# Kernel optimization log

Measured on AMD Instinct MI355X. Metric: run time of the kernel, lower is better.

## Reference

```python
import jax, jax.numpy as jnp
import numpy as np

N, F, S, D, H, K, L = 6000, 16, 64, 256, 8, 32, 2
DH = D // H
NEG = jnp.float32(-1e9)


def _ln(x, g, b, eps=1e-5):
    m = jnp.mean(x, axis=-1, keepdims=True)
    v = jnp.var(x, axis=-1, keepdims=True)
    return (x - m) * jax.lax.rsqrt(v + eps) * g + b


def _gelu(x):
    return jax.nn.gelu(x, approximate=False)  # torch nn.GELU default = exact erf


def setup_inputs() -> dict:
    keys = iter(jax.random.split(jax.random.key(0), 64))

    def p(*shape):
        return jax.random.normal(next(keys), shape, jnp.float32) * 0.02

    return dict(
        x=jax.random.normal(next(keys), (N, F, S), jnp.float32),
        gru_Wih=p(F, 3 * D, S), gru_bih=p(F, 3 * D), gru_bhh=p(F, 3 * D),
        va_Wq=p(L, D, D), va_bq=p(L, D), va_Wk=p(L, D, D), va_bk=p(L, D),
        va_Wv=p(L, D, D), va_bv=p(L, D),
        va_lnq_g=jnp.ones((L, D)), va_lnq_b=jnp.zeros((L, D)),
        va_lnk_g=jnp.ones((L, D)), va_lnk_b=jnp.zeros((L, D)),
        va_lnv_g=jnp.ones((L, D)), va_lnv_b=jnp.zeros((L, D)),
        va_Wo=p(L, D, D), va_bo=p(L, D),
        va_ln_g=jnp.ones((L, D)), va_ln_b=jnp.zeros((L, D)),
        va_fi_W1=p(L, D, D), va_fi_b1=p(L, D), va_fi_W2=p(L, D), va_fi_b2=p(L),
        gat_W=p(3, D, D), gat_asrc=p(3, H, DH), gat_adst=p(3, H, DH), gat_bias=p(3, D),
        imp_W=p(3, D), imp_b=p(3),
        ga_ln_g=jnp.ones((D,)), ga_ln_b=jnp.zeros((D,)),
        fin_ln_g=jnp.ones((D,)), fin_ln_b=jnp.zeros((D,)),
        pred_W1=p(D, 2 * D), pred_b1=p(2 * D), pred_W2=p(2 * D), pred_b2=p(),
    )


def _gat(x, W, asrc, adst, bias, src, tgt, valid):
    # PyG GATConv (concat heads, leaky_relu slope 0.2); messages flow src -> tgt.
    # PyG removes then re-adds self loops; `valid` masks removed self-duplicates,
    # the last N edges are the re-added self loops.
    h = (x @ W).reshape(N, H, DH)                              # [N,H,DH]
    es = jnp.einsum('nhd,hd->nh', h, asrc)
    ed = jnp.einsum('nhd,hd->nh', h, adst)
    e = jax.nn.leaky_relu(es[src] + ed[tgt], 0.2)              # [E,H]
    e = jnp.where(valid[:, None], e, NEG)
    m = jax.ops.segment_max(e, tgt, num_segments=N)            # [N,H]
    p = jnp.where(valid[:, None], jnp.exp(e - m[tgt]), 0.0)
    s = jax.ops.segment_sum(p, tgt, num_segments=N)
    alpha = p / (s[tgt] + 1e-16)                               # segment softmax
    out = jax.ops.segment_sum(alpha[:, :, None] * h[src], tgt, num_segments=N)
    return out.reshape(N, D) + bias


def _forward(x, gru_Wih, gru_bih, gru_bhh, va_Wq, va_bq, va_Wk, va_bk, va_Wv, va_bv,
             va_lnq_g, va_lnq_b, va_lnk_g, va_lnk_b, va_lnv_g, va_lnv_b,
             va_Wo, va_bo, va_ln_g, va_ln_b, va_fi_W1, va_fi_b1, va_fi_W2, va_fi_b2,
             gat_W, gat_asrc, gat_adst, gat_bias, imp_W, imp_b,
             ga_ln_g, ga_ln_b, fin_ln_g, fin_ln_b, pred_W1, pred_b1, pred_W2, pred_b2):
    # --- TimeMixing ('gru'): single-step GRU cell per feature, h0 = 0 (torch gate order r,z,n)
    g = jnp.einsum('nfs,fks->nfk', x, gru_Wih) + gru_bih       # [N,F,3D]
    gr, gz, gn = jnp.split(g, 3, axis=-1)
    br, bz, bn = jnp.split(gru_bhh, 3, axis=-1)
    r = jax.nn.sigmoid(gr + br)
    z = jax.nn.sigmoid(gz + bz)
    emb = (1.0 - z) * jnp.tanh(gn + r * bn)                    # [N,F,D]

    # --- VariableAttentionLayers (attention over the F feature tokens, batch = nodes)
    scale = 1.0 / np.sqrt(DH)
    fi = None
    for l in range(L):
        xo = emb
        q = _ln(emb @ va_Wq[l] + va_bq[l], va_lnq_g[l], va_lnq_b[l]).reshape(N, F, H, DH)
        kk = _ln(emb @ va_Wk[l] + va_bk[l], va_lnk_g[l], va_lnk_b[l]).reshape(N, F, H, DH)
        vv = _ln(emb @ va_Wv[l] + va_bv[l], va_lnv_g[l], va_lnv_b[l]).reshape(N, F, H, DH)
        A = jax.nn.softmax(jnp.einsum('bche,bshe->bhcs', q, kk) * scale, axis=-1)
        o = jnp.einsum('bhcs,bshd->bchd', A, vv).reshape(N, F, D) @ va_Wo[l] + va_bo[l]
        emb = _ln(_gelu(o) + xo, va_ln_g[l], va_ln_b[l])
        w = _gelu(emb @ va_fi_W1[l] + va_fi_b1[l]) @ va_fi_W2[l] + va_fi_b2[l]  # [N,F]
        fi = jax.nn.softmax(w, axis=1)[..., None]              # softmax over features

    # --- FeatureImportanceTokenizedBlock
    node = jnp.sum(fi * emb, axis=1)                           # [N,D]

    # --- top-k / bottom-k neighbor selection (cosine similarity, self excluded)
    xn = node * jax.lax.rsqrt(jnp.sum(node * node, axis=-1, keepdims=True) + 1e-12)
    sim = xn @ xn.T                                            # [N,N]
    diag = jnp.eye(N, dtype=bool)
    _, top_idx = jax.lax.top_k(jnp.where(diag, NEG, sim), K)   # [N,K]
    _, bot_idx = jax.lax.top_k(jnp.where(diag, NEG, -sim), K)  # [N,K]

    rng = jnp.arange(N)

    def edges(idx):
        s0 = jnp.repeat(rng, K)
        t0 = idx.reshape(-1)
        src = jnp.concatenate([s0, rng])
        tgt = jnp.concatenate([t0, rng])
        valid = jnp.concatenate([s0 != t0, jnp.ones((N,), bool)])
        return src, tgt, valid

    # --- GatedAttentionLayer: self GAT has only self loops -> attention weight = 1
    self_out = node @ gat_W[0] + gat_bias[0]
    s1, t1, m1 = edges(top_idx)
    top_out = _gat(node, gat_W[1], gat_asrc[1], gat_adst[1], gat_bias[1], s1, t1, m1)
    s2, t2, m2 = edges(bot_idx)
    bot_out = _gat(node, gat_W[2], gat_asrc[2], gat_adst[2], gat_bias[2], s2, t2, m2)

    logits = jnp.stack([self_out @ imp_W[0] + imp_b[0],
                        top_out @ imp_W[1] + imp_b[1],
                        bot_out @ imp_W[2] + imp_b[2]], axis=-1)  # [N,3]
    iw = jax.nn.softmax(logits, axis=-1)
    fused = iw[:, 0:1] * self_out + iw[:, 1:2] * top_out + iw[:, 2:3] * bot_out
    out = _ln(_gelu(fused) + node, ga_ln_g, ga_ln_b)

    # --- final norm + predictor
    out = _ln(out, fin_ln_g, fin_ln_b)
    pred = _gelu(out @ pred_W1 + pred_b1) @ pred_W2 + pred_b2
    return pred[:, None]                                       # [N,1]


def reference(x, gru_Wih, gru_bih, gru_bhh, va_Wq, va_bq, va_Wk, va_bk, va_Wv, va_bv,
              va_lnq_g, va_lnq_b, va_lnk_g, va_lnk_b, va_lnv_g, va_lnv_b,
              va_Wo, va_bo, va_ln_g, va_ln_b, va_fi_W1, va_fi_b1, va_fi_W2, va_fi_b2,
              gat_W, gat_asrc, gat_adst, gat_bias, imp_W, imp_b,
              ga_ln_g, ga_ln_b, fin_ln_g, fin_ln_b, pred_W1, pred_b1, pred_W2, pred_b2):
    return _forward(x, gru_Wih, gru_bih, gru_bhh, va_Wq, va_bq, va_Wk, va_bk, va_Wv, va_bv,
                    va_lnq_g, va_lnq_b, va_lnk_g, va_lnk_b, va_lnv_g, va_lnv_b,
                    va_Wo, va_bo, va_ln_g, va_ln_b, va_fi_W1, va_fi_b1, va_fi_W2, va_fi_b2,
                    gat_W, gat_asrc, gat_adst, gat_bias, imp_W, imp_b,
                    ga_ln_g, ga_ln_b, fin_ln_g, fin_ln_b, pred_W1, pred_b1, pred_W2, pred_b2)
```

## Files before the change

### kernel.cpp

```cpp
#include <hip/hip_runtime.h>
#include <hip/hip_bf16.h>
#include <math.h>

#define N_  6000
#define F_  16
#define S_  64
#define D_  256
#define H_  8
#define KK_ 32
#define L_  2
#define DH_ 32
#define E_  (N_*KK_ + N_)
#define NF_ (N_*F_)

typedef float f32x4 __attribute__((ext_vector_type(4)));
typedef float f32v4 __attribute__((ext_vector_type(4)));
typedef __bf16 bf16_t;
typedef bf16_t bf16x8 __attribute__((ext_vector_type(8)));


__device__ __forceinline__ float geluf(float x) {
  return 0.5f * x * (1.0f + erff(x * 0.7071067811865476f));
}
__device__ __forceinline__ float sigmf(float x) {
  return 1.0f / (1.0f + expf(-x));
}
__device__ __forceinline__ float block_sum_256(float v, float* red) {
  int tid = threadIdx.x;
  red[tid] = v; __syncthreads();
  #pragma unroll
  for (int s = 128; s > 0; s >>= 1) {
    if (tid < s) red[tid] += red[tid + s];
    __syncthreads();
  }
  float r = red[0];
  __syncthreads();
  return r;
}
__device__ __forceinline__ unsigned fmap(float f) {
  unsigned u = __float_as_uint(f);
  return (u & 0x80000000u) ? ~u : (u | 0x80000000u);
}
__device__ __forceinline__ float funmap(unsigned u) {
  unsigned b = (u & 0x80000000u) ? (u ^ 0x80000000u) : ~u;
  return __uint_as_float(b);
}

__global__ void transpose12_kernel(const float* s0, const float* s1, const float* s2,
                                   const float* s3, const float* s4, const float* s5,
                                   const float* s6, const float* s7, const float* s8,
                                   const float* s9, const float* s10, const float* s11,
                                   __hip_bfloat16* __restrict__ dst) {
  int m = blockIdx.y;
  const float* src;
  switch (m) {
    case 0: src = s0; break; case 1: src = s1; break; case 2: src = s2; break;
    case 3: src = s3; break; case 4: src = s4; break; case 5: src = s5; break;
    case 6: src = s6; break; case 7: src = s7; break; case 8: src = s8; break;
    case 9: src = s9; break; case 10: src = s10; break; default: src = s11; break;
  }
  int o = blockIdx.x, i = threadIdx.x;
  dst[(size_t)m * 65536 + o * 256 + i] = __float2bfloat16(src[(size_t)i * 256 + o]);
}
__global__ void transpose_pred_kernel(const float* __restrict__ src, __hip_bfloat16* __restrict__ dst) {
  int o = blockIdx.x, i = threadIdx.x;
  dst[(size_t)o * 256 + i] = __float2bfloat16(src[(size_t)i * 512 + o]);
}
__global__ void biascat_kernel(const float* __restrict__ bq, const float* __restrict__ bk,
                               const float* __restrict__ bv, float* __restrict__ dst) {
  int s = blockIdx.x, l = blockIdx.y, t = threadIdx.x;
  const float* p = (s == 0) ? bq : (s == 1) ? bk : bv;
  dst[l * 768 + s * 256 + t] = p[l * 256 + t];
}
__global__ void gatbias_kernel(const float* __restrict__ gb, float* __restrict__ b3) {
  int t = blockIdx.x * 256 + threadIdx.x;
  if (t < 768) b3[t] = (t < 256) ? gb[t] : 0.f;
}
__global__ void gruw_cvt_kernel(const float* __restrict__ Wih,
                                __hip_bfloat16* __restrict__ Wh) {
  size_t idx = (size_t)blockIdx.x * 256 + threadIdx.x;
  Wh[idx] = __float2bfloat16(Wih[idx]);
}
__global__ void zero_f_kernel(float* __restrict__ p, int n) {
  int i = blockIdx.x * 256 + threadIdx.x;
  if (i < n) p[i] = 0.f;
}
__global__ void init_scalar_kernel(float* __restrict__ p, const float* __restrict__ s, int n) {
  int i = blockIdx.x * 256 + threadIdx.x;
  if (i < n) p[i] = s[0];
}

__global__ __launch_bounds__(256)
void gru_mfma_kernel(const float* __restrict__ x,
                     const __hip_bfloat16* __restrict__ Wh,
                     const float* __restrict__ bih, const float* __restrict__ bhh,
                     float* __restrict__ emb) {
  __shared__ __align__(16) __hip_bfloat16 Ash[64 * 32];
  __shared__ __align__(16) __hip_bfloat16 Bsh[384 * 32];
  int kb = blockIdx.x, rb = blockIdx.y, f = blockIdx.z;
  int tid = threadIdx.x;
  int lane = tid & 63, wid = tid >> 6;
  int wrow = (wid & 1) * 32, wcol = (wid >> 1) * 64;
  int q = lane >> 4, m16 = lane & 15;

  f32x4 aR[2][4], aZ[2][4], aN[2][4];
  #pragma unroll
  for (int i = 0; i < 2; i++)
    #pragma unroll
    for (int j = 0; j < 4; j++) {
      aR[i][j] = (f32x4){0.f,0.f,0.f,0.f};
      aZ[i][j] = (f32x4){0.f,0.f,0.f,0.f};
      aN[i][j] = (f32x4){0.f,0.f,0.f,0.f};
    }

  for (int k0 = 0; k0 < 64; k0 += 32) {
    {
      int r = tid >> 2, ch = tid & 3;
      int gn = rb * 64 + r;
      bool ok = gn < N_;
      const float* src = x + ((size_t)gn * F_ + f) * S_ + k0 + ch * 8;
      union { __hip_bfloat16 h[8]; uint4 u; } t8;
      #pragma unroll
      for (int v = 0; v < 2; v++) {
        f32v4 d = ok ? *reinterpret_cast<const f32v4*>(src + v * 4) : (f32v4){0.f,0.f,0.f,0.f};
        t8.h[v * 4 + 0] = __float2bfloat16(d.x);
        t8.h[v * 4 + 1] = __float2bfloat16(d.y);
        t8.h[v * 4 + 2] = __float2bfloat16(d.z);
        t8.h[v * 4 + 3] = __float2bfloat16(d.w);
      }
      *reinterpret_cast<uint4*>(&Ash[r * 32 + (ch ^ (r & 3)) * 8]) = t8.u;
    }
    #pragma unroll
    for (int i = 0; i < 6; i++) {
      int cid = tid + i * 256;
      int row = cid >> 2, ch = cid & 3;
      size_t roff = ((size_t)f * 768 + (row >> 7) * 256 + kb * 128 + (row & 127)) * S_ + k0 + ch * 8;
      uint4 v = *reinterpret_cast<const uint4*>(Wh + roff);
      *reinterpret_cast<uint4*>(&Bsh[row * 32 + (ch ^ (row & 3)) * 8]) = v;
    }
    __syncthreads();
    bf16x8 ah[2];
    #pragma unroll
    for (int mt = 0; mt < 2; mt++) {
      int ar = wrow + mt * 16 + m16;
      ah[mt] = *reinterpret_cast<const bf16x8*>(&Ash[ar * 32 + (q ^ (ar & 3)) * 8]);
    }
    #pragma unroll
    for (int g = 0; g < 3; g++) {
      bf16x8 bh[4];
      #pragma unroll
      for (int nt = 0; nt < 4; nt++) {
        int br = g * 128 + wcol + nt * 16 + m16;
        bh[nt] = *reinterpret_cast<const bf16x8*>(&Bsh[br * 32 + (q ^ (br & 3)) * 8]);
      }
      #pragma unroll
      for (int mt = 0; mt < 2; mt++)
        #pragma unroll
        for (int nt = 0; nt < 4; nt++) {
          f32x4 acc = (g == 0) ? aR[mt][nt] : (g == 1) ? aZ[mt][nt] : aN[mt][nt];
          acc = __builtin_amdgcn_mfma_f32_16x16x32_bf16(ah[mt], bh[nt], acc, 0, 0, 0);
          if (g == 0) aR[mt][nt] = acc; else if (g == 1) aZ[mt][nt] = acc; else aN[mt][nt] = acc;
        }
    }
    __syncthreads();
  }
  #pragma unroll
  for (int mt = 0; mt < 2; mt++)
    #pragma unroll
    for (int nt = 0; nt < 4; nt++) {
      int k = kb * 128 + wcol + nt * 16 + m16;
      float brc = bih[f * 768 + k]       + bhh[f * 768 + k];
      float bzc = bih[f * 768 + 256 + k] + bhh[f * 768 + 256 + k];
      float bni = bih[f * 768 + 512 + k];
      float bnh = bhh[f * 768 + 512 + k];
      #pragma unroll
      for (int r4 = 0; r4 < 4; r4++) {
        int gn = rb * 64 + wrow + mt * 16 + q * 4 + r4;
        if (gn < N_) {
          float rr = sigmf(aR[mt][nt][r4] + brc);
          float zz = sigmf(aZ[mt][nt][r4] + bzc);
          float nn = tanhf(aN[mt][nt][r4] + bni + rr * bnh);
          emb[((size_t)gn * F_ + f) * D_ + k] = (1.f - zz) * nn;
        }
      }
    }
}

__global__ __launch_bounds__(256)
void qkv_attn_kernel(const float* __restrict__ emb, const __hip_bfloat16* __restrict__ Wt,
                     const float* __restrict__ bias, __hip_bfloat16* __restrict__ out,
                     const float* __restrict__ gq, const float* __restrict__ bq,
                     const float* __restrict__ gk, const float* __restrict__ bk,
                     const float* __restrict__ gv, const float* __restrict__ bv) {
  __shared__ __align__(16) __hip_bfloat16 As[16 * 256];
  __shared__ __align__(16) unsigned char shbuf[16 * 772 * 4];
  __hip_bfloat16* Bs = reinterpret_cast<__hip_bfloat16*>(shbuf);
  float (*tile)[772] = reinterpret_cast<float (*)[772]>(shbuf);
  int n = blockIdx.x, tid = threadIdx.x;
  int lane = tid & 63, w = tid >> 6;
  int q = lane >> 4, m16 = lane & 15;

  #pragma unroll
  for (int i = 0; i < 2; i++) {
    int cid = tid + i * 256;
    int r = cid >> 5, ch = cid & 31;
    const float* src = emb + ((size_t)n * 16 + r) * 256 + ch * 8;
    union { __hip_bfloat16 h[8]; uint4 u; } t8;
    #pragma unroll
    for (int v = 0; v < 2; v++) {
      f32v4 d = *reinterpret_cast<const f32v4*>(src + v * 4);
      t8.h[v * 4 + 0] = __float2bfloat16(d.x);
      t8.h[v * 4 + 1] = __float2bfloat16(d.y);
      t8.h[v * 4 + 2] = __float2bfloat16(d.z);
      t8.h[v * 4 + 3] = __float2bfloat16(d.w);
    }
    *reinterpret_cast<uint4*>(&As[r * 256 + (ch ^ (r & 7)) * 8]) = t8.u;
  }

  f32x4 acc[12];
  #pragma unroll
  for (int j = 0; j < 12; j++) acc[j] = (f32x4){0.f,0.f,0.f,0.f};
  for (int k = 0; k < 8; k++) {
    __syncthreads();
    #pragma unroll
    for (int i = 0; i < 12; i++) {
      int cid = tid + i * 256;
      int row = cid >> 2, ch = cid & 3;
      uint4 v = *reinterpret_cast<const uint4*>(Wt + (size_t)row * 256 + k * 32 + ch * 8);
      *reinterpret_cast<uint4*>(&Bs[row * 32 + (ch ^ (row & 3)) * 8]) = v;
    }
    __syncthreads();
    int c = k * 4 + q;
    bf16x8 a = *reinterpret_cast<const bf16x8*>(&As[m16 * 256 + (c ^ (m16 & 7)) * 8]);
    #pragma unroll
    for (int j = 0; j < 12; j++) {
      int br = (w * 12 + j) * 16 + m16;
      bf16x8 b = *reinterpret_cast<const bf16x8*>(&Bs[br * 32 + (q ^ (br & 3)) * 8]);
      acc[j] = __builtin_amdgcn_mfma_f32_16x16x32_bf16(a, b, acc[j], 0, 0, 0);
    }
  }
  __syncthreads();

  #pragma unroll
  for (int j = 0; j < 12; j++) {
    int col = (w * 12 + j) * 16 + m16;
    float bc = bias[col];
    #pragma unroll
    for (int r = 0; r < 4; r++)
      tile[q * 4 + r][col] = acc[j][r] + bc;
  }
  __syncthreads();

  for (int ii = 0; ii < 12; ii++) {
    int sl = w * 12 + ii;
    int s = sl >> 4, f = sl & 15;
    float* p = &tile[f][s * 256];
    float4 d = *reinterpret_cast<float4*>(p + lane * 4);
    float sum = d.x + d.y + d.z + d.w;
    #pragma unroll
    for (int m = 1; m < 64; m <<= 1) sum += __shfl_xor(sum, m, 64);
    float mean = sum * (1.f / 256.f);
    float e0 = d.x - mean, e1 = d.y - mean, e2 = d.z - mean, e3 = d.w - mean;
    float sq = e0 * e0 + e1 * e1 + e2 * e2 + e3 * e3;
    #pragma unroll
    for (int m = 1; m < 64; m <<= 1) sq += __shfl_xor(sq, m, 64);
    float inv = rsqrtf(sq * (1.f / 256.f) + 1e-5f);
    const float* g  = (s == 0) ? gq : (s == 1) ? gk : gv;
    const float* bb = (s == 0) ? bq : (s == 1) ? bk : bv;
    float4 gg = *reinterpret_cast<const float4*>(g + lane * 4);
    float4 bo = *reinterpret_cast<const float4*>(bb + lane * 4);
    d.x = e0 * inv * gg.x + bo.x;
    d.y = e1 * inv * gg.y + bo.y;
    d.z = e2 * inv * gg.z + bo.z;
    d.w = e3 * inv * gg.w + bo.w;
    *reinterpret_cast<float4*>(p + lane * 4) = d;
  }
  __syncthreads();

  int c = tid & 15, h = (tid >> 4) & 7, half = tid >> 7;
  const float scale = 0.17677669529663687f;
  float sc[16];
  float mx = -3e38f;
  #pragma unroll
  for (int s = 0; s < 16; s++) {
    float a2 = 0.f;
    #pragma unroll
    for (int e = 0; e < 32; e++)
      a2 += tile[c][h * 32 + e] * tile[s][256 + h * 32 + e];
    sc[s] = a2 * scale;
    mx = fmaxf(mx, sc[s]);
  }
  float sum = 0.f;
  #pragma unroll
  for (int s = 0; s < 16; s++) { sc[s] = expf(sc[s] - mx); sum += sc[s]; }
  float inv = 1.f / sum;
  #pragma unroll
  for (int dd = 0; dd < 16; dd++) {
    int d = half * 16 + dd;
    float a2 = 0.f;
    #pragma unroll
    for (int s = 0; s < 16; s++) a2 += sc[s] * tile[s][512 + h * 32 + d];
    out[((size_t)n * 16 + c) * 256 + h * 32 + d] = __float2bfloat16(a2 * inv);
  }
}

template <int EPI>
__global__ __launch_bounds__(256)
void gemm_fA_bB(const float* __restrict__ A, const __hip_bfloat16* __restrict__ Btb,
                const float* __restrict__ bias, float* __restrict__ C,
                int M, int K, int Nt) {
  __shared__ __align__(16) __hip_bfloat16 As[128 * 32];
  __shared__ __align__(16) __hip_bfloat16 Bs[128 * 32];
  int mb = blockIdx.y * 128, nb = blockIdx.x * 128;
  int tid = threadIdx.x;
  int lane = tid & 63, wid = tid >> 6;
  int wm = (wid >> 1) * 64, wn = (wid & 1) * 64;
  int q = lane >> 4, m16 = lane & 15;
  int arow = tid >> 1;
  int acol = (tid & 1) * 16;

  f32x4 acc[4][4];
  #pragma unroll
  for (int i = 0; i < 4; i++)
    #pragma unroll
    for (int j = 0; j < 4; j++) acc[i][j] = (f32x4){0.f, 0.f, 0.f, 0.f};

  uint4 z4 = {0u,0u,0u,0u};
  for (int k0 = 0; k0 < K; k0 += 32) {
    {
      bool ok = (mb + arow) < M;
      const float* src = A + (size_t)(mb + arow) * K + k0 + acol;
      union { __hip_bfloat16 h[16]; uint4 u[2]; } tmp;
      #pragma unroll
      for (int v = 0; v < 4; v++) {
        f32v4 d = ok ? *reinterpret_cast<const f32v4*>(src + v * 4) : (f32v4){0.f,0.f,0.f,0.f};
        tmp.h[v * 4 + 0] = __float2bfloat16(d.x);
        tmp.h[v * 4 + 1] = __float2bfloat16(d.y);
        tmp.h[v * 4 + 2] = __float2bfloat16(d.z);
        tmp.h[v * 4 + 3] = __float2bfloat16(d.w);
      }
      uint4* dst = reinterpret_cast<uint4*>(&As[arow * 32 + acol]);
      dst[0] = tmp.u[0]; dst[1] = tmp.u[1];
    }
    {
      bool ok = (nb + arow) < Nt;
      const uint4* src = reinterpret_cast<const uint4*>(Btb + (size_t)(nb + arow) * K + k0 + acol);
      uint4* dst = reinterpret_cast<uint4*>(&Bs[arow * 32 + acol]);
      dst[0] = ok ? src[0] : z4; dst[1] = ok ? src[1] : z4;
    }
    __syncthreads();
    bf16x8 av[4], bv[4];
    #pragma unroll
    for (int mt = 0; mt < 4; mt++)
      av[mt] = *reinterpret_cast<const bf16x8*>(&As[(wm + mt * 16 + m16) * 32 + q * 8]);
    #pragma unroll
    for (int nt = 0; nt < 4; nt++)
      bv[nt] = *reinterpret_cast<const bf16x8*>(&Bs[(wn + nt * 16 + m16) * 32 + q * 8]);
    #pragma unroll
    for (int mt = 0; mt < 4; mt++)
      #pragma unroll
      for (int nt = 0; nt < 4; nt++)
        acc[mt][nt] = __builtin_amdgcn_mfma_f32_16x16x32_bf16(av[mt], bv[nt], acc[mt][nt], 0, 0, 0);
    __syncthreads();
  }
  #pragma unroll
  for (int mt = 0; mt < 4; mt++) {
    #pragma unroll
    for (int nt = 0; nt < 4; nt++) {
      #pragma unroll
      for (int r = 0; r < 4; r++) {
        int row = mb + wm + mt * 16 + q * 4 + r;
        int col = nb + wn + nt * 16 + m16;
        if (row < M && col < Nt) {
          float c = acc[mt][nt][r] + (bias ? bias[col] : 0.f);
          if (EPI == 1) c = geluf(c);
          C[(size_t)row * Nt + col] = c;
        }
      }
    }
  }
}

__global__ __launch_bounds__(256)
void gemm_dot2(const float* __restrict__ A, const __hip_bfloat16* __restrict__ Btb,
               const float* __restrict__ bias, const float* __restrict__ w2,
               float* __restrict__ out1, int M, int K, int Nt) {
  __shared__ __align__(16) __hip_bfloat16 As[128 * 32];
  __shared__ __align__(16) __hip_bfloat16 Bs[128 * 32];
  int mb = blockIdx.y * 128, nb = blockIdx.x * 128;
  int tid = threadIdx.x;
  int lane = tid & 63, wid = tid >> 6;
  int wm = (wid >> 1) * 64, wn = (wid & 1) * 64;
  int q = lane >> 4, m16 = lane & 15;
  int arow = tid >> 1;
  int acol = (tid & 1) * 16;

  f32x4 acc[4][4];
  #pragma unroll
  for (int i = 0; i < 4; i++)
    #pragma unroll
    for (int j = 0; j < 4; j++) acc[i][j] = (f32x4){0.f, 0.f, 0.f, 0.f};

  uint4 z4 = {0u,0u,0u,0u};
  for (int k0 = 0; k0 < K; k0 += 32) {
    {
      bool ok = (mb + arow) < M;
      const float* src = A + (size_t)(mb + arow) * K + k0 + acol;
      union { __hip_bfloat16 h[16]; uint4 u[2]; } tmp;
      #pragma unroll
      for (int v = 0; v < 4; v++) {
        f32v4 d = ok ? *reinterpret_cast<const f32v4*>(src + v * 4) : (f32v4){0.f,0.f,0.f,0.f};
        tmp.h[v * 4 + 0] = __float2bfloat16(d.x);
        tmp.h[v * 4 + 1] = __float2bfloat16(d.y);
        tmp.h[v * 4 + 2] = __float2bfloat16(d.z);
        tmp.h[v * 4 + 3] = __float2bfloat16(d.w);
      }
      uint4* dst = reinterpret_cast<uint4*>(&As[arow * 32 + acol]);
      dst[0] = tmp.u[0]; dst[1] = tmp.u[1];
    }
    {
      bool ok = (nb + arow) < Nt;
      const uint4* src = reinterpret_cast<const uint4*>(Btb + (size_t)(nb + arow) * K + k0 + acol);
      uint4* dst = reinterpret_cast<uint4*>(&Bs[arow * 32 + acol]);
      dst[0] = ok ? src[0] : z4; dst[1] = ok ? src[1] : z4;
    }
    __syncthreads();
    bf16x8 av[4], bv[4];
    #pragma unroll
    for (int mt = 0; mt < 4; mt++)
      av[mt] = *reinterpret_cast<const bf16x8*>(&As[(wm + mt * 16 + m16) * 32 + q * 8]);
    #pragma unroll
    for (int nt = 0; nt < 4; nt++)
      bv[nt] = *reinterpret_cast<const bf16x8*>(&Bs[(wn + nt * 16 + m16) * 32 + q * 8]);
    #pragma unroll
    for (int mt = 0; mt < 4; mt++)
      #pragma unroll
      for (int nt = 0; nt < 4; nt++)
        acc[mt][nt] = __builtin_amdgcn_mfma_f32_16x16x32_bf16(av[mt], bv[nt], acc[mt][nt], 0, 0, 0);
    __syncthreads();
  }
  #pragma unroll
  for (int mt = 0; mt < 4; mt++) {
    #pragma unroll
    for (int r = 0; r < 4; r++) {
      int row = mb + wm + mt * 16 + q * 4 + r;
      float s = 0.f;
      #pragma unroll
      for (int nt = 0; nt < 4; nt++) {
        int col = nb + wn + nt * 16 + m16;
        float c = geluf(acc[mt][nt][r] + bias[col]);
        s += c * w2[col];
      }
      #pragma unroll
      for (int m = 1; m < 16; m <<= 1) s += __shfl_xor(s, m, 64);
      if (m16 == 0 && row < M) atomicAdd(&out1[row], s);
    }
  }
}

__global__ __launch_bounds__(256)
void wo_resid_ln_kernel(const __hip_bfloat16* __restrict__ A, const __hip_bfloat16* __restrict__ Btb,
                        const float* __restrict__ bias, float* __restrict__ emb,
                        const float* __restrict__ g, const float* __restrict__ b, int M) {
  __shared__ __align__(16) __hip_bfloat16 As[64 * 32];
  __shared__ __align__(16) __hip_bfloat16 Bs[256 * 32];
  int mb = blockIdx.x * 64;
  int tid = threadIdx.x, lane = tid & 63, w = tid >> 6;
  int q = lane >> 4, m16 = lane & 15;
  f32x4 acc[16];
  #pragma unroll
  for (int nt = 0; nt < 16; nt++) acc[nt] = (f32x4){0.f,0.f,0.f,0.f};
  uint4 z4 = {0u,0u,0u,0u};
  for (int k0 = 0; k0 < 256; k0 += 32) {
    { int r = tid >> 2, c0 = (tid & 3) * 8;
      int gr = mb + r;
      uint4 v = (gr < M) ? *reinterpret_cast<const uint4*>(A + (size_t)gr * 256 + k0 + c0) : z4;
      *reinterpret_cast<uint4*>(&As[r * 32 + c0]) = v; }
    { const uint4* src = reinterpret_cast<const uint4*>(Btb + (size_t)tid * 256 + k0);
      uint4* dst = reinterpret_cast<uint4*>(&Bs[tid * 32]);
      dst[0] = src[0]; dst[1] = src[1]; dst[2] = src[2]; dst[3] = src[3]; }
    __syncthreads();
    bf16x8 av = *reinterpret_cast<const bf16x8*>(&As[(w * 16 + m16) * 32 + q * 8]);
    #pragma unroll
    for (int nt = 0; nt < 16; nt++) {
      bf16x8 bv = *reinterpret_cast<const bf16x8*>(&Bs[(nt * 16 + m16) * 32 + q * 8]);
      acc[nt] = __builtin_amdgcn_mfma_f32_16x16x32_bf16(av, bv, acc[nt], 0, 0, 0);
    }
    __syncthreads();
  }
  #pragma unroll
  for (int r = 0; r < 4; r++) {
    int grow = mb + w * 16 + q * 4 + r;
    if (grow >= M) continue;
    float s = 0.f;
    #pragma unroll
    for (int nt = 0; nt < 16; nt++) {
      int col = nt * 16 + m16;
      float v = geluf(acc[nt][r] + bias[col]) + emb[(size_t)grow * 256 + col];
      acc[nt][r] = v; s += v;
    }
    #pragma unroll
    for (int m = 1; m < 16; m <<= 1) s += __shfl_xor(s, m, 64);
    float mean = s * (1.f / 256.f);
    float sq = 0.f;
    #pragma unroll
    for (int nt = 0; nt < 16; nt++) { float d = acc[nt][r] - mean; sq += d * d; }
    #pragma unroll
    for (int m = 1; m < 16; m <<= 1) sq += __shfl_xor(sq, m, 64);
    float inv = rsqrtf(sq * (1.f / 256.f) + 1e-5f);
    #pragma unroll
    for (int nt = 0; nt < 16; nt++) {
      int col = nt * 16 + m16;
      emb[(size_t)grow * 256 + col] = (acc[nt][r] - mean) * inv * g[col] + b[col];
    }
  }
}

__global__ __launch_bounds__(256)
void sim_split_kernel(const __hip_bfloat16* __restrict__ xh, const __hip_bfloat16* __restrict__ xl,
                      float* __restrict__ C) {
  __shared__ __align__(16) __hip_bfloat16 Ah[128 * 32];
  __shared__ __align__(16) __hip_bfloat16 Al[128 * 32];
  __shared__ __align__(16) __hip_bfloat16 Bh[128 * 32];
  __shared__ __align__(16) __hip_bfloat16 Bl[128 * 32];
  int mb = blockIdx.y * 128, nb = blockIdx.x * 128;
  int tid = threadIdx.x;
  int lane = tid & 63, wid = tid >> 6;
  int wm = (wid >> 1) * 64, wn = (wid & 1) * 64;
  int q = lane >> 4, m16 = lane & 15;
  int row = tid >> 1, halfk = (tid & 1) * 16;

  f32x4 acc[4][4];
  #pragma unroll
  for (int i = 0; i < 4; i++)
    #pragma unroll
    for (int j = 0; j < 4; j++) acc[i][j] = (f32x4){0.f, 0.f, 0.f, 0.f};

  uint4 z = {0u, 0u, 0u, 0u};
  for (int k0 = 0; k0 < 256; k0 += 32) {
    {
      int gr = mb + row; bool ok = gr < N_;
      const uint4* sh = reinterpret_cast<const uint4*>(xh + (size_t)gr * 256 + k0 + halfk);
      const uint4* sl = reinterpret_cast<const uint4*>(xl + (size_t)gr * 256 + k0 + halfk);
      uint4* dh = reinterpret_cast<uint4*>(&Ah[row * 32 + halfk]);
      uint4* dl = reinterpret_cast<uint4*>(&Al[row * 32 + halfk]);
      dh[0] = ok ? sh[0] : z; dh[1] = ok ? sh[1] : z;
      dl[0] = ok ? sl[0] : z; dl[1] = ok ? sl[1] : z;
    }
    {
      int gc = nb + row; bool ok = gc < N_;
      const uint4* sh = reinterpret_cast<const uint4*>(xh + (size_t)gc * 256 + k0 + halfk);
      const uint4* sl = reinterpret_cast<const uint4*>(xl + (size_t)gc * 256 + k0 + halfk);
      uint4* dh = reinterpret_cast<uint4*>(&Bh[row * 32 + halfk]);
      uint4* dl = reinterpret_cast<uint4*>(&Bl[row * 32 + halfk]);
      dh[0] = ok ? sh[0] : z; dh[1] = ok ? sh[1] : z;
      dl[0] = ok ? sl[0] : z; dl[1] = ok ? sl[1] : z;
    }
    __syncthreads();
    bf16x8 avh[4], avl[4], bvh[4], bvl[4];
    #pragma unroll
    for (int mt = 0; mt < 4; mt++) {
      avh[mt] = *reinterpret_cast<const bf16x8*>(&Ah[(wm + mt * 16 + m16) * 32 + q * 8]);
      avl[mt] = *reinterpret_cast<const bf16x8*>(&Al[(wm + mt * 16 + m16) * 32 + q * 8]);
    }
    #pragma unroll
    for (int nt = 0; nt < 4; nt++) {
      bvh[nt] = *reinterpret_cast<const bf16x8*>(&Bh[(wn + nt * 16 + m16) * 32 + q * 8]);
      bvl[nt] = *reinterpret_cast<const bf16x8*>(&Bl[(wn + nt * 16 + m16) * 32 + q * 8]);
    }
    #pragma unroll
    for (int mt = 0; mt < 4; mt++)
      #pragma unroll
      for (int nt = 0; nt < 4; nt++) {
        acc[mt][nt] = __builtin_amdgcn_mfma_f32_16x16x32_bf16(avh[mt], bvh[nt], acc[mt][nt], 0, 0, 0);
        acc[mt][nt] = __builtin_amdgcn_mfma_f32_16x16x32_bf16(avh[mt], bvl[nt], acc[mt][nt], 0, 0, 0);
        acc[mt][nt] = __builtin_amdgcn_mfma_f32_16x16x32_bf16(avl[mt], bvh[nt], acc[mt][nt], 0, 0, 0);
      }
    __syncthreads();
  }
  #pragma unroll
  for (int mt = 0; mt < 4; mt++)
    #pragma unroll
    for (int nt = 0; nt < 4; nt++)
      #pragma unroll
      for (int r = 0; r < 4; r++) {
        int rr = mb + wm + mt * 16 + q * 4 + r;
        int cc = nb + wn + nt * 16 + m16;
        if (rr < N_ && cc < N_) C[(size_t)rr * N_ + cc] = acc[mt][nt][r];
      }
}

__global__ __launch_bounds__(256)
void node_prep_kernel(const float* __restrict__ wbuf, const float* __restrict__ emb,
                      float* __restrict__ node, __hip_bfloat16* __restrict__ xh,
                      __hip_bfloat16* __restrict__ xl) {
  __shared__ float wsh[16];
  __shared__ float red[256];
  int n = blockIdx.x, tid = threadIdx.x;
  if (tid < 16) wsh[tid] = wbuf[n * 16 + tid];
  __syncthreads();
  float mx = -3e38f;
  #pragma unroll
  for (int f = 0; f < 16; f++) mx = fmaxf(mx, wsh[f]);
  float e[16], ssum = 0.f;
  #pragma unroll
  for (int f = 0; f < 16; f++) { e[f] = expf(wsh[f] - mx); ssum += e[f]; }
  float inv = 1.f / ssum;
  float acc = 0.f;
  #pragma unroll
  for (int f = 0; f < 16; f++)
    acc += e[f] * emb[((size_t)n * 16 + f) * 256 + tid];
  acc *= inv;
  node[(size_t)n * 256 + tid] = acc;
  float ss = block_sum_256(acc * acc, red);
  float y = acc * rsqrtf(ss + 1e-12f);
  __hip_bfloat16 h = __float2bfloat16(y);
  xh[(size_t)n * 256 + tid] = h;
  xl[(size_t)n * 256 + tid] = __float2bfloat16(y - __bfloat162float(h));
}

__global__ __launch_bounds__(256)
void topk_kernel(const float* __restrict__ sim, int* __restrict__ top,
                 int* __restrict__ bot) {
  __shared__ unsigned wsum[2][4];
  __shared__ unsigned short tie[1024];
  __shared__ unsigned s_out, s_tcnt;
  int i = blockIdx.x, tid = threadIdx.x;
  int lane = tid & 63, wid = tid >> 6;
  unsigned raw[24];
  unsigned validmask = 0;
  #pragma unroll
  for (int k = 0; k < 24; k++) {
    int j = tid + k * 256;
    bool ok = (j < N_) && (j != i);
    raw[k] = ok ? fmap(sim[(size_t)i * N_ + j]) : 0u;
    validmask |= (ok ? 1u : 0u) << k;
  }
  unsigned match_t = validmask, match_b = validmask;
  unsigned sel_t = 0, sel_b = 0;
  unsigned r_t = KK_, r_b = KK_;
  bool act_t = true, act_b = true;
  for (int bit = 31; bit >= 0; bit--) {
    unsigned bmask = 0;
    #pragma unroll
    for (int k = 0; k < 24; k++) bmask |= ((raw[k] >> bit) & 1u) << k;
    unsigned effb = (~bmask) & 0x00ffffffu;
    unsigned packed = (unsigned)__popc(match_t & bmask) |
                      ((unsigned)__popc(match_b & effb) << 16);
    #pragma unroll
    for (int m = 1; m < 64; m <<= 1) packed += (unsigned)__shfl_xor((int)packed, m, 64);
    if (lane == 0) wsum[bit & 1][wid] = packed;
    __syncthreads();
    unsigned tot = wsum[bit & 1][0] + wsum[bit & 1][1] + wsum[bit & 1][2] + wsum[bit & 1][3];
    unsigned tt = tot & 0xffffu, tb = tot >> 16;
    if (act_t) {
      if (tt >= r_t) {
        match_t &= bmask;
        if (tt == r_t) { sel_t |= match_t; act_t = false; }
      } else { sel_t |= match_t & bmask; r_t -= tt; match_t &= ~bmask; }
    }
    if (act_b) {
      if (tb >= r_b) {
        match_b &= effb;
        if (tb == r_b) { sel_b |= match_b; act_b = false; }
      } else { sel_b |= match_b & effb; r_b -= tb; match_b &= ~effb; }
    }
    if (!(act_t || act_b)) break;
  }
  for (int pass = 0; pass < 2; pass++) {
    int* dst = pass ? bot : top;
    unsigned sel = pass ? sel_b : sel_t;
    unsigned match = pass ? match_b : match_t;
    bool act = pass ? act_b : act_t;
    unsigned r = pass ? r_b : r_t;
    if (tid == 0) { s_out = 0; s_tcnt = 0; }
    __syncthreads();
    unsigned s = sel;
    while (s) {
      int k = __ffs(s) - 1; s &= s - 1;
      unsigned p = atomicAdd(&s_out, 1u);
      dst[i * KK_ + p] = tid + k * 256;
    }
    if (act) {
      unsigned m0 = match;
      while (m0) {
        int k = __ffs(m0) - 1; m0 &= m0 - 1;
        unsigned qx = atomicAdd(&s_tcnt, 1u);
        if (qx < 1024u) tie[qx] = (unsigned short)(tid + k * 256);
      }
    }
    __syncthreads();
    if (act) {
      int tcnt = (int)min(s_tcnt, 1024u);
      int basep = KK_ - (int)r;
      int last = -1;
      for (int t = 0; t < (int)r; t++) {
        unsigned best = 0xffffffffu;
        for (int idx = tid; idx < tcnt; idx += 256) {
          int j = (int)tie[idx];
          if (j > last && (unsigned)j < best) best = (unsigned)j;
        }
        #pragma unroll
        for (int m = 1; m < 64; m <<= 1) best = min(best, (unsigned)__shfl_xor((int)best, m, 64));
        if (lane == 0) wsum[t & 1][wid] = best;
        __syncthreads();
        best = min(min(wsum[t & 1][0], wsum[t & 1][1]), min(wsum[t & 1][2], wsum[t & 1][3]));
        last = (int)best;
        if (tid == 0) dst[i * KK_ + basep + t] = last;
        __syncthreads();
      }
    }
    __syncthreads();
  }
}

__device__ __forceinline__ void edge_decode(int e, const int* nbr, int& src, int& tgt, bool& valid) {
  if (e < N_ * KK_) { src = e >> 5; tgt = nbr[e]; valid = (src != tgt); }
  else { src = tgt = e - N_ * KK_; valid = true; }
}

__global__ void gat_esed2_kernel(const float* __restrict__ gout, const float* __restrict__ asrc,
                                 const float* __restrict__ adst,
                                 float* __restrict__ es, float* __restrict__ ed) {
  int idx = blockIdx.x * 256 + threadIdx.x;
  if (idx >= 2 * N_ * H_) return;
  int g = idx / (N_ * H_), r = idx - g * (N_ * H_);
  int hh = r & 7, node = r >> 3;
  const float* hp = gout + 256 + 256 * g + (size_t)node * 768 + hh * 32;
  const float* as = asrc + 256 + 256 * g + hh * 32;
  const float* ad = adst + 256 + 256 * g + hh * 32;
  float a = 0.f, b = 0.f;
  for (int d = 0; d < 32; d++) { float hv = hp[d]; a += hv * as[d]; b += hv * ad[d]; }
  es[idx] = a; ed[idx] = b;
}

__global__ void gat_init2_kernel(unsigned* __restrict__ mu, float* __restrict__ sb,
                                 float* __restrict__ tobo) {
  int idx = blockIdx.x * 256 + threadIdx.x;
  if (idx < 2 * N_ * H_) { mu[idx] = fmap(-1e9f); sb[idx] = 0.f; }
  if (idx < 2 * N_ * D_) tobo[idx] = 0.f;
}

__global__ void gat_edge_max2_kernel(const int* __restrict__ topi, const int* __restrict__ boti,
                                     const float* __restrict__ es, const float* __restrict__ ed,
                                     unsigned* __restrict__ mu) {
  int t = blockIdx.x * 256 + threadIdx.x;
  if (t >= 2 * E_ * H_) return;
  int g = t / (E_ * H_), r = t - g * (E_ * H_);
  int e = r >> 3, hh = r & 7;
  const int* nbr = g ? boti : topi;
  int src, tgt; bool valid;
  edge_decode(e, nbr, src, tgt, valid);
  float ev = -1e9f;
  if (valid) {
    float xv = es[g * N_ * H_ + src * 8 + hh] + ed[g * N_ * H_ + tgt * 8 + hh];
    ev = xv > 0.f ? xv : 0.2f * xv;
  }
  atomicMax(&mu[g * N_ * H_ + tgt * 8 + hh], fmap(ev));
}

__global__ void gat_edge_sum2_kernel(const int* __restrict__ topi, const int* __restrict__ boti,
                                     const float* __restrict__ es, const float* __restrict__ ed,
                                     const unsigned* __restrict__ mu, float* __restrict__ sb,
                                     float* __restrict__ p) {
  int t = blockIdx.x * 256 + threadIdx.x;
  if (t >= 2 * E_ * H_) return;
  int g = t / (E_ * H_), r = t - g * (E_ * H_);
  int e = r >> 3, hh = r & 7;
  const int* nbr = g ? boti : topi;
  int src, tgt; bool valid;
  edge_decode(e, nbr, src, tgt, valid);
  float pv = 0.f;
  if (valid) {
    float xv = es[g * N_ * H_ + src * 8 + hh] + ed[g * N_ * H_ + tgt * 8 + hh];
    float ev = xv > 0.f ? xv : 0.2f * xv;
    pv = expf(ev - funmap(mu[g * N_ * H_ + tgt * 8 + hh]));
  }
  p[t] = pv;
  if (pv != 0.f) atomicAdd(&sb[g * N_ * H_ + tgt * 8 + hh], pv);
}

__global__ void csr_zero2_kernel(int* __restrict__ deg) {
  int i = blockIdx.x * 256 + threadIdx.x;
  if (i < 2 * N_) deg[i] = 0;
}
__global__ void csr_count2_kernel(const int* __restrict__ topi, const int* __restrict__ boti,
                                  int* __restrict__ deg) {
  int e2 = blockIdx.x * 256 + threadIdx.x;
  if (e2 >= 2 * E_) return;
  int g = e2 / E_, e = e2 - g * E_;
  const int* nbr = g ? boti : topi;
  int src, tgt; bool valid;
  edge_decode(e, nbr, src, tgt, valid);
  if (valid) atomicAdd(&deg[g * N_ + tgt], 1);
}
__global__ __launch_bounds__(256)
void csr_scan2_kernel(const int* __restrict__ deg, int* __restrict__ off, int* __restrict__ cur) {
  __shared__ int red[256];
  int tid = threadIdx.x;
  int base = tid * 47;
  int loc[47];
  int s = 0;
  for (int k = 0; k < 47; k++) {
    int i = base + k;
    int v = (i < 2 * N_) ? deg[i] : 0;
    loc[k] = s; s += v;
  }
  red[tid] = s; __syncthreads();
  int total = s;
  for (int st = 1; st < 256; st <<= 1) {
    int add = (tid >= st) ? red[tid - st] : 0;
    __syncthreads();
    red[tid] += add;
    __syncthreads();
  }
  int texcl = red[tid] - total;
  for (int k = 0; k < 47; k++) {
    int i = base + k;
    if (i < 2 * N_) { int o = texcl + loc[k]; off[i] = o; cur[i] = o; }
  }
  if (tid == 255) off[2 * N_] = red[255];
}
__global__ void csr_scatter2_kernel(const int* __restrict__ topi, const int* __restrict__ boti,
                                    int* __restrict__ cur, int* __restrict__ eidx,
                                    int* __restrict__ tidx) {
  int e2 = blockIdx.x * 256 + threadIdx.x;
  if (e2 >= 2 * E_) return;
  int g = e2 / E_, e = e2 - g * E_;
  const int* nbr = g ? boti : topi;
  int src, tgt; bool valid;
  edge_decode(e, nbr, src, tgt, valid);
  if (valid) { int pos = atomicAdd(&cur[g * N_ + tgt], 1); eidx[pos] = e2; tidx[pos] = g * N_ + tgt; }
}

__global__ __launch_bounds__(256)
void gat_seg2_kernel(const int* __restrict__ off2N, const int* __restrict__ eidx,
                     const int* __restrict__ tidx, const float* __restrict__ p,
                     const float* __restrict__ sb, const float* __restrict__ gout,
                     float* __restrict__ tobo) {
  __shared__ int se[64], st[64];
  int total = off2N[0];
  int b0 = blockIdx.x * 64;
  if (b0 >= total) return;
  int cnt = min(64, total - b0);
  int tid = threadIdx.x;
  if (tid < cnt) { se[tid] = eidx[b0 + tid]; st[tid] = tidx[b0 + tid]; }
  __syncthreads();
  int hh = tid >> 5;
  float acc = 0.f;
  int curT = st[0];
  for (int ii = 0; ii < cnt; ii++) {
    int tg = st[ii];
    if (tg != curT) {
      float invS = 1.f / (sb[curT * 8 + hh] + 1e-16f);
      atomicAdd(&tobo[(size_t)curT * 256 + tid], acc * invS);
      acc = 0.f; curT = tg;
    }
    int e2 = se[ii];
    int g = (e2 >= E_) ? 1 : 0;
    int e = e2 - g * E_;
    int src = (e < N_ * KK_) ? (e >> 5) : (e - N_ * KK_);
    float pv = p[(size_t)e2 * 8 + hh];
    acc += pv * gout[256 + 256 * g + (size_t)src * 768 + tid];
  }
  float invS = 1.f / (sb[curT * 8 + hh] + 1e-16f);
  atomicAdd(&tobo[(size_t)curT * 256 + tid], acc * invS);
}

__global__ __launch_bounds__(256)
void fuse_kernel(const float* __restrict__ so, const float* __restrict__ to,
                 const float* __restrict__ bo, const float* __restrict__ gatb,
                 const float* __restrict__ impW, const float* __restrict__ impb,
                 const float* __restrict__ node,
                 const float* __restrict__ gag, const float* __restrict__ gab,
                 const float* __restrict__ fing, const float* __restrict__ finb,
                 float* __restrict__ outv, int ldso) {
  __shared__ float red[256];
  size_t row = blockIdx.x;
  int tid = threadIdx.x;
  float s0 = so[row * ldso + tid];
  float t0 = to[row * 256 + tid] + gatb[256 + tid];
  float b0 = bo[row * 256 + tid] + gatb[512 + tid];
  float l0 = block_sum_256(s0 * impW[tid], red) + impb[0];
  float l1 = block_sum_256(t0 * impW[256 + tid], red) + impb[1];
  float l2 = block_sum_256(b0 * impW[512 + tid], red) + impb[2];
  float mx = fmaxf(l0, fmaxf(l1, l2));
  float e0 = expf(l0 - mx), e1 = expf(l1 - mx), e2 = expf(l2 - mx);
  float inv = 1.f / (e0 + e1 + e2);
  float fused = (e0 * s0 + e1 * t0 + e2 * b0) * inv;
  float v = geluf(fused) + node[row * 256 + tid];
  float mean = block_sum_256(v, red) * (1.f / 256.f);
  float d = v - mean;
  float var = block_sum_256(d * d, red) * (1.f / 256.f);
  float y = d * rsqrtf(var + 1e-5f) * gag[tid] + gab[tid];
  mean = block_sum_256(y, red) * (1.f / 256.f);
  d = y - mean;
  var = block_sum_256(d * d, red) * (1.f / 256.f);
  outv[row * 256 + tid] = d * rsqrtf(var + 1e-5f) * fing[tid] + finb[tid];
}

extern "C" void kernel_launch(void* const* d_in, const int* in_sizes, int n_in,
                              void* d_out, int out_size, void* d_ws, size_t ws_size,
                              hipStream_t stream) {
  const float* x        = (const float*)d_in[0];
  const float* gru_Wih  = (const float*)d_in[1];
  const float* gru_bih  = (const float*)d_in[2];
  const float* gru_bhh  = (const float*)d_in[3];
  const float* va_Wq    = (const float*)d_in[4];
  const float* va_bq    = (const float*)d_in[5];
  const float* va_Wk    = (const float*)d_in[6];
  const float* va_bk    = (const float*)d_in[7];
  const float* va_Wv    = (const float*)d_in[8];
  const float* va_bv    = (const float*)d_in[9];
  const float* va_lnq_g = (const float*)d_in[10];
  const float* va_lnq_b = (const float*)d_in[11];
  const float* va_lnk_g = (const float*)d_in[12];
  const float* va_lnk_b = (const float*)d_in[13];
  const float* va_lnv_g = (const float*)d_in[14];
  const float* va_lnv_b = (const float*)d_in[15];
  const float* va_Wo    = (const float*)d_in[16];
  const float* va_bo    = (const float*)d_in[17];
  const float* va_ln_g  = (const float*)d_in[18];
  const float* va_ln_b  = (const float*)d_in[19];
  const float* va_fi_W1 = (const float*)d_in[20];
  const float* va_fi_b1 = (const float*)d_in[21];
  const float* va_fi_W2 = (const float*)d_in[22];
  const float* va_fi_b2 = (const float*)d_in[23];
  const float* gat_W    = (const float*)d_in[24];
  const float* gat_asrc = (const float*)d_in[25];
  const float* gat_adst = (const float*)d_in[26];
  const float* gat_bias = (const float*)d_in[27];
  const float* imp_W    = (const float*)d_in[28];
  const float* imp_b    = (const float*)d_in[29];
  const float* ga_ln_g  = (const float*)d_in[30];
  const float* ga_ln_b  = (const float*)d_in[31];
  const float* fin_ln_g = (const float*)d_in[32];
  const float* fin_ln_b = (const float*)d_in[33];
  const float* pred_W1  = (const float*)d_in[34];
  const float* pred_b1  = (const float*)d_in[35];
  const float* pred_W2  = (const float*)d_in[36];
  const float* pred_b2  = (const float*)d_in[37];

  float* base   = (float*)d_ws;
  float* emb    = base;
  __hip_bfloat16* obuf = (__hip_bfloat16*)(base + 24576000);
  float* smalls = base + 36864000;
  float* wbuf   = smalls;
  float* nodeb  = smalls + 192000;
  __hip_bfloat16* xh = (__hip_bfloat16*)(smalls + 1728000);
  __hip_bfloat16* xl = (__hip_bfloat16*)(smalls + 2496000);
  int*   topi   = (int*)(smalls + 3264000);
  int*   boti   = (int*)(smalls + 3456000);
  float* wtb    = smalls + 3648000;
  float* simb   = base;
  float* gout   = base + 0;
  float* to     = base + 4608000;
  float* bo     = base + 6144000;
  float* esb    = base + 7680000;
  float* edb    = base + 7776000;
  unsigned* mu  = (unsigned*)(base + 7872000);
  float* sb     = base + 7968000;
  float* pb     = base + 8064000;
  float* outv   = base + 11232000;
  int* csr_off  = (int*)(base + 12768000);
  int* csr_cur  = (int*)(base + 12782000);
  int* csr_deg  = (int*)(base + 12794000);
  int* csr_eidx = (int*)(base + 12806000);
  int* csr_tidx = (int*)(base + 13202000);

  __hip_bfloat16* wbf    = (__hip_bfloat16*)wtb;
  __hip_bfloat16* predtb = (__hip_bfloat16*)(wtb + 393216);
  float* qkvb   = wtb + 458752;
  float* b3     = wtb + 460288;
  __hip_bfloat16* gwh = (__hip_bfloat16*)(wtb + 461056);

  transpose12_kernel<<<dim3(256, 12), 256, 0, stream>>>(
      va_Wq, va_Wk, va_Wv, va_Wq + 65536, va_Wk + 65536, va_Wv + 65536,
      va_Wo, va_Wo + 65536, va_fi_W1 + (L_-1) * 65536,
      gat_W, gat_W + 65536, gat_W + 131072, wbf);
  transpose_pred_kernel<<<512, 256, 0, stream>>>(pred_W1, predtb);
  biascat_kernel<<<dim3(3, 2), 256, 0, stream>>>(va_bq, va_bk, va_bv, qkvb);
  gatbias_kernel<<<3, 256, 0, stream>>>(gat_bias, b3);
  gruw_cvt_kernel<<<3072, 256, 0, stream>>>(gru_Wih, gwh);

  gru_mfma_kernel<<<dim3(2, 94, 16), 256, 0, stream>>>(x, gwh, gru_bih, gru_bhh, emb);

  for (int l = 0; l < L_; l++) {
    const __hip_bfloat16* qkvtb = wbf + (size_t)l * 3 * 65536;
    const __hip_bfloat16* wotb  = wbf + (size_t)(6 + l) * 65536;
    qkv_attn_kernel<<<N_, 256, 0, stream>>>(emb, qkvtb, qkvb + l * 768, obuf,
                                            va_lnq_g + l * 256, va_lnq_b + l * 256,
                                            va_lnk_g + l * 256, va_lnk_b + l * 256,
                                            va_lnv_g + l * 256, va_lnv_b + l * 256);
    wo_resid_ln_kernel<<<(NF_ + 63) / 64, 256, 0, stream>>>(obuf, wotb, va_bo + l * 256,
                                                            emb, va_ln_g + l * 256,
                                                            va_ln_b + l * 256, NF_);
  }

  zero_f_kernel<<<(NF_ + 255) / 256, 256, 0, stream>>>(wbuf, NF_);
  gemm_dot2<<<dim3(2, (NF_ + 127) / 128), 256, 0, stream>>>(emb, wbf + 8 * 65536,
                                                            va_fi_b1 + (L_-1) * 256,
                                                            va_fi_W2 + (L_-1) * 256,
                                                            wbuf, NF_, 256, 256);
  node_prep_kernel<<<N_, 256, 0, stream>>>(wbuf, emb, nodeb, xh, xl);

  sim_split_kernel<<<dim3(47, 47), 256, 0, stream>>>(xh, xl, simb);
  topk_kernel<<<N_, 256, 0, stream>>>(simb, topi, boti);

  gemm_fA_bB<0><<<dim3(6, 47), 256, 0, stream>>>(nodeb, wbf + 9 * 65536, b3, gout, N_, 256, 768);

  const int G_NH2 = (2 * N_ * H_ + 255) / 256;
  const int G_ND2 = (2 * N_ * D_ + 255) / 256;
  const int G_EH2 = (2 * E_ * H_ + 255) / 256;
  const int G_E2  = (2 * E_ + 255) / 256;
  const int G_SEG = (2 * E_ + 63) / 64;
  gat_esed2_kernel<<<G_NH2, 256, 0, stream>>>(gout, gat_asrc, gat_adst, esb, edb);
  gat_init2_kernel<<<G_ND2, 256, 0, stream>>>(mu, sb, to);
  gat_edge_max2_kernel<<<G_EH2, 256, 0, stream>>>(topi, boti, esb, edb, mu);
  gat_edge_sum2_kernel<<<G_EH2, 256, 0, stream>>>(topi, boti, esb, edb, mu, sb, pb);
  csr_zero2_kernel<<<(2 * N_ + 255) / 256, 256, 0, stream>>>(csr_deg);
  csr_count2_kernel<<<G_E2, 256, 0, stream>>>(topi, boti, csr_deg);
  csr_scan2_kernel<<<1, 256, 0, stream>>>(csr_deg, csr_off, csr_cur);
  csr_scatter2_kernel<<<G_E2, 256, 0, stream>>>(topi, boti, csr_cur, csr_eidx, csr_tidx);
  gat_seg2_kernel<<<G_SEG, 256, 0, stream>>>(csr_off + 2 * N_, csr_eidx, csr_tidx, pb, sb,
                                             gout, to);

  fuse_kernel<<<N_, 256, 0, stream>>>(gout, to, bo, gat_bias, imp_W, imp_b, nodeb,
                                      ga_ln_g, ga_ln_b, fin_ln_g, fin_ln_b, outv, 768);

  init_scalar_kernel<<<(N_ + 255) / 256, 256, 0, stream>>>((float*)d_out, pred_b2, N_);
  gemm_dot2<<<dim3(4, 47), 256, 0, stream>>>(outv, predtb, pred_b1, pred_W2,
                                             (float*)d_out, N_, 256, 512);
}
```

Measured before the change: 1.728 ms.

## Process two nodes per block in QKV attention kernel to reuse weight tiles

Each block of the fused QKV projection and attention kernel now handles two nodes (32 rows) instead of one. Every staged weight tile feeds two MFMA rows, so global weight traffic per node is halved. The B shared tile switches from an XOR swizzle to a padded stride. The cost is double the accumulator registers (24 f32x4) and a serial epilogue per node, which may lower occupancy.

```diff
diff --git a/kernel.cpp b/kernel.cpp
--- a/kernel.cpp
+++ b/kernel.cpp
@@ -186,25 +186,26 @@
     }
 }
 
+#define BSTRIDE 40
 __global__ __launch_bounds__(256)
-void qkv_attn_kernel(const float* __restrict__ emb, const __hip_bfloat16* __restrict__ Wt,
-                     const float* __restrict__ bias, __hip_bfloat16* __restrict__ out,
-                     const float* __restrict__ gq, const float* __restrict__ bq,
-                     const float* __restrict__ gk, const float* __restrict__ bk,
-                     const float* __restrict__ gv, const float* __restrict__ bv) {
-  __shared__ __align__(16) __hip_bfloat16 As[16 * 256];
-  __shared__ __align__(16) unsigned char shbuf[16 * 772 * 4];
+void qkv_attn2_kernel(const float* __restrict__ emb, const __hip_bfloat16* __restrict__ Wt,
+                      const float* __restrict__ bias, __hip_bfloat16* __restrict__ out,
+                      const float* __restrict__ gq, const float* __restrict__ bq,
+                      const float* __restrict__ gk, const float* __restrict__ bk,
+                      const float* __restrict__ gv, const float* __restrict__ bv) {
+  __shared__ __align__(16) __hip_bfloat16 As[32 * 256];
+  __shared__ __align__(16) unsigned char shbuf[768 * BSTRIDE * 2];
   __hip_bfloat16* Bs = reinterpret_cast<__hip_bfloat16*>(shbuf);
   float (*tile)[772] = reinterpret_cast<float (*)[772]>(shbuf);
-  int n = blockIdx.x, tid = threadIdx.x;
+  int n0 = blockIdx.x * 2, tid = threadIdx.x;
   int lane = tid & 63, w = tid >> 6;
   int q = lane >> 4, m16 = lane & 15;
 
   #pragma unroll
-  for (int i = 0; i < 2; i++) {
+  for (int i = 0; i < 4; i++) {
     int cid = tid + i * 256;
     int r = cid >> 5, ch = cid & 31;
-    const float* src = emb + ((size_t)n * 16 + r) * 256 + ch * 8;
+    const float* src = emb + ((size_t)n0 * 16 + r) * 256 + ch * 8;
     union { __hip_bfloat16 h[8]; uint4 u; } t8;
     #pragma unroll
     for (int v = 0; v < 2; v++) {
@@ -217,9 +218,11 @@
     *reinterpret_cast<uint4*>(&As[r * 256 + (ch ^ (r & 7)) * 8]) = t8.u;
   }
 
-  f32x4 acc[12];
-  #pragma unroll
-  for (int j = 0; j < 12; j++) acc[j] = (f32x4){0.f,0.f,0.f,0.f};
+  f32x4 acc[2][12];
+  #pragma unroll
+  for (int mi = 0; mi < 2; mi++)
+    #pragma unroll
+    for (int j = 0; j < 12; j++) acc[mi][j] = (f32x4){0.f,0.f,0.f,0.f};
   for (int k = 0; k < 8; k++) {
     __syncthreads();
     #pragma unroll
@@ -227,80 +230,84 @@
       int cid = tid + i * 256;
       int row = cid >> 2, ch = cid & 3;
       uint4 v = *reinterpret_cast<const uint4*>(Wt + (size_t)row * 256 + k * 32 + ch * 8);
-      *reinterpret_cast<uint4*>(&Bs[row * 32 + (ch ^ (row & 3)) * 8]) = v;
+      *reinterpret_cast<uint4*>(&Bs[row * BSTRIDE + ch * 8]) = v;
     }
     __syncthreads();
     int c = k * 4 + q;
-    bf16x8 a = *reinterpret_cast<const bf16x8*>(&As[m16 * 256 + (c ^ (m16 & 7)) * 8]);
+    bf16x8 a0 = *reinterpret_cast<const bf16x8*>(&As[m16 * 256 + (c ^ (m16 & 7)) * 8]);
+    bf16x8 a1 = *reinterpret_cast<const bf16x8*>(&As[(16 + m16) * 256 + (c ^ (m16 & 7)) * 8]);
     #pragma unroll
     for (int j = 0; j < 12; j++) {
       int br = (w * 12 + j) * 16 + m16;
-      bf16x8 b = *reinterpret_cast<const bf16x8*>(&Bs[br * 32 + (q ^ (br & 3)) * 8]);
-      acc[j] = __builtin_amdgcn_mfma_f32_16x16x32_bf16(a, b, acc[j], 0, 0, 0);
-    }
-  }
-  __syncthreads();
-
-  #pragma unroll
-  for (int j = 0; j < 12; j++) {
-    int col = (w * 12 + j) * 16 + m16;
-    float bc = bias[col];
-    #pragma unroll
-    for (int r = 0; r < 4; r++)
-      tile[q * 4 + r][col] = acc[j][r] + bc;
-  }
-  __syncthreads();
-
-  for (int ii = 0; ii < 12; ii++) {
-    int sl = w * 12 + ii;
-    int s = sl >> 4, f = sl & 15;
-    float* p = &tile[f][s * 256];
-    float4 d = *reinterpret_cast<float4*>(p + lane * 4);
-    float sum = d.x + d.y + d.z + d.w;
-    #pragma unroll
-    for (int m = 1; m < 64; m <<= 1) sum += __shfl_xor(sum, m, 64);
-    float mean = sum * (1.f / 256.f);
-    float e0 = d.x - mean, e1 = d.y - mean, e2 = d.z - mean, e3 = d.w - mean;
-    float sq = e0 * e0 + e1 * e1 + e2 * e2 + e3 * e3;
-    #pragma unroll
-    for (int m = 1; m < 64; m <<= 1) sq += __shfl_xor(sq, m, 64);
-    float inv = rsqrtf(sq * (1.f / 256.f) + 1e-5f);
-    const float* g  = (s == 0) ? gq : (s == 1) ? gk : gv;
-    const float* bb = (s == 0) ? bq : (s == 1) ? bk : bv;
-    float4 gg = *reinterpret_cast<const float4*>(g + lane * 4);
-    float4 bo = *reinterpret_cast<const float4*>(bb + lane * 4);
-    d.x = e0 * inv * gg.x + bo.x;
-    d.y = e1 * inv * gg.y + bo.y;
-    d.z = e2 * inv * gg.z + bo.z;
-    d.w = e3 * inv * gg.w + bo.w;
-    *reinterpret_cast<float4*>(p + lane * 4) = d;
-  }
-  __syncthreads();
-
-  int c = tid & 15, h = (tid >> 4) & 7, half = tid >> 7;
-  const float scale = 0.17677669529663687f;
-  float sc[16];
-  float mx = -3e38f;
-  #pragma unroll
-  for (int s = 0; s < 16; s++) {
-    float a2 = 0.f;
-    #pragma unroll
-    for (int e = 0; e < 32; e++)
-      a2 += tile[c][h * 32 + e] * tile[s][256 + h * 32 + e];
-    sc[s] = a2 * scale;
-    mx = fmaxf(mx, sc[s]);
-  }
-  float sum = 0.f;
-  #pragma unroll
-  for (int s = 0; s < 16; s++) { sc[s] = expf(sc[s] - mx); sum += sc[s]; }
-  float inv = 1.f / sum;
-  #pragma unroll
-  for (int dd = 0; dd < 16; dd++) {
-    int d = half * 16 + dd;
-    float a2 = 0.f;
-    #pragma unroll
-    for (int s = 0; s < 16; s++) a2 += sc[s] * tile[s][512 + h * 32 + d];
-    out[((size_t)n * 16 + c) * 256 + h * 32 + d] = __float2bfloat16(a2 * inv);
+      bf16x8 b = *reinterpret_cast<const bf16x8*>(&Bs[br * BSTRIDE + q * 8]);
+      acc[0][j] = __builtin_amdgcn_mfma_f32_16x16x32_bf16(a0, b, acc[0][j], 0, 0, 0);
+      acc[1][j] = __builtin_amdgcn_mfma_f32_16x16x32_bf16(a1, b, acc[1][j], 0, 0, 0);
+    }
+  }
+
+  for (int mi = 0; mi < 2; mi++) {
+    __syncthreads();
+    #pragma unroll
+    for (int j = 0; j < 12; j++) {
+      int col = (w * 12 + j) * 16 + m16;
+      float bc = bias[col];
+      #pragma unroll
+      for (int r = 0; r < 4; r++)
+        tile[q * 4 + r][col] = acc[mi][j][r] + bc;
+    }
+    __syncthreads();
+
+    for (int ii = 0; ii < 12; ii++) {
+      int sl = w * 12 + ii;
+      int s = sl >> 4, f = sl & 15;
+      float* p = &tile[f][s * 256];
+      float4 d = *reinterpret_cast<float4*>(p + lane * 4);
+      float sum = d.x + d.y + d.z + d.w;
+      #pragma unroll
+      for (int m = 1; m < 64; m <<= 1) sum += __shfl_xor(sum, m, 64);
+      float mean = sum * (1.f / 256.f);
+      float e0 = d.x - mean, e1 = d.y - mean, e2 = d.z - mean, e3 = d.w - mean;
+      float sq = e0 * e0 + e1 * e1 + e2 * e2 + e3 * e3;
+      #pragma unroll
+      for (int m = 1; m < 64; m <<= 1) sq += __shfl_xor(sq, m, 64);
+      float inv = rsqrtf(sq * (1.f / 256.f) + 1e-5f);
+      const float* g  = (s == 0) ? gq : (s == 1) ? gk : gv;
+      const float* bb = (s == 0) ? bq : (s == 1) ? bk : bv;
+      float4 gg = *reinterpret_cast<const float4*>(g + lane * 4);
+      float4 bo = *reinterpret_cast<const float4*>(bb + lane * 4);
+      d.x = e0 * inv * gg.x + bo.x;
+      d.y = e1 * inv * gg.y + bo.y;
+      d.z = e2 * inv * gg.z + bo.z;
+      d.w = e3 * inv * gg.w + bo.w;
+      *reinterpret_cast<float4*>(p + lane * 4) = d;
+    }
+    __syncthreads();
+
+    int c = tid & 15, h = (tid >> 4) & 7, half = tid >> 7;
+    const float scale = 0.17677669529663687f;
+    float sc[16];
+    float mx = -3e38f;
+    #pragma unroll
+    for (int s = 0; s < 16; s++) {
+      float a2 = 0.f;
+      #pragma unroll
+      for (int e = 0; e < 32; e++)
+        a2 += tile[c][h * 32 + e] * tile[s][256 + h * 32 + e];
+      sc[s] = a2 * scale;
+      mx = fmaxf(mx, sc[s]);
+    }
+    float sum = 0.f;
+    #pragma unroll
+    for (int s = 0; s < 16; s++) { sc[s] = expf(sc[s] - mx); sum += sc[s]; }
+    float inv = 1.f / sum;
+    #pragma unroll
+    for (int dd = 0; dd < 16; dd++) {
+      int d = half * 16 + dd;
+      float a2 = 0.f;
+      #pragma unroll
+      for (int s = 0; s < 16; s++) a2 += sc[s] * tile[s][512 + h * 32 + d];
+      out[((size_t)(n0 + mi) * 16 + c) * 256 + h * 32 + d] = __float2bfloat16(a2 * inv);
+    }
   }
 }
 
@@ -988,10 +995,10 @@
   for (int l = 0; l < L_; l++) {
     const __hip_bfloat16* qkvtb = wbf + (size_t)l * 3 * 65536;
     const __hip_bfloat16* wotb  = wbf + (size_t)(6 + l) * 65536;
-    qkv_attn_kernel<<<N_, 256, 0, stream>>>(emb, qkvtb, qkvb + l * 768, obuf,
-                                            va_lnq_g + l * 256, va_lnq_b + l * 256,
-                                            va_lnk_g + l * 256, va_lnk_b + l * 256,
-                                            va_lnv_g + l * 256, va_lnv_b + l * 256);
+    qkv_attn2_kernel<<<N_ / 2, 256, 0, stream>>>(emb, qkvtb, qkvb + l * 768, obuf,
+                                                 va_lnq_g + l * 256, va_lnq_b + l * 256,
+                                                 va_lnk_g + l * 256, va_lnk_b + l * 256,
+                                                 va_lnv_g + l * 256, va_lnv_b + l * 256);
     wo_resid_ln_kernel<<<(NF_ + 63) / 64, 256, 0, stream>>>(obuf, wotb, va_bo + l * 256,
                                                             emb, va_ln_g + l * 256,
                                                             va_ln_b + l * 256, NF_);
```

After: 2.167 ms. +25.4%, slower.
